# Optimization experiments

Hardware: AMD Instinct MI355X
Metric: run time of the kernel (lower is better)

Reference implementation:

```python
import jax, jax.numpy as jnp
import numpy as np

B, DX, DS, H, K, NSN = 1048576, 32, 16, 128, 64, 4

def setup_inputs() -> dict:
    key = jax.random.key(0)
    ks = jax.random.split(key, 9)
    return {
        "x": jax.random.normal(ks[0], (B, DX), jnp.float32),
        "s": jax.random.normal(ks[1], (B, DS), jnp.float32),
        "hidden": jax.random.normal(ks[2], (B, H), jnp.float32),
        "naive_pred": jax.random.normal(ks[3], (B, 1), jnp.float32),
        # learned parameters
        "centers": jax.random.normal(ks[4], (K, DX), jnp.float32),
        "W_tune": jax.random.normal(ks[5], (H, 1), jnp.float32) * 0.05,
        "b_tune": jnp.zeros((1,), jnp.float32),
        "W_sn": jax.random.normal(ks[6], (NSN, K, DS), jnp.float32) * 0.1,
        "b_sn": jax.random.normal(ks[7], (NSN, K), jnp.float32) * 0.1,
        "running_sn_weight": jnp.full((K, NSN), 1.0 / NSN, jnp.float32),
    }

def reference(x, s, hidden, naive_pred, centers, W_tune, b_tune, W_sn, b_sn, running_sn_weight):
    # tune head: linear -> sigmoid, [B,1]
    x_tune = jax.nn.sigmoid(hidden @ W_tune + b_tune)
    # nearest-centroid clustering: argmin ||x - c_k||^2 (||x||^2 dropped, constant per row)
    dist = jnp.sum(centers * centers, axis=1) - 2.0 * (x @ centers.T)  # [B,K]
    x_cluster = jnp.argmin(dist, axis=1)  # [B] int32
    # sub-networks: per-cluster linear heads on s; gather cluster-indexed weights
    Ws = W_sn[:, x_cluster, :]                                   # [NSN,B,DS] gather
    x_sn = jnp.einsum('nbd,bd->bn', Ws, s) + b_sn[:, x_cluster].T  # [B,NSN]
    # indexed weighted reduction over sub-network outputs
    w = running_sn_weight[x_cluster]                             # [B,NSN] gather
    x_sn_sum = jnp.sum(x_sn * w, axis=1, keepdims=True)          # [B,1]
    out = x_sn_sum + x_tune * (naive_pred - x_sn_sum)
    return out
```

## Files before the change

kernel.cpp:

```cpp
#include <hip/hip_runtime.h>
#include <math.h>

#define DXc 32
#define DSc 16
#define Hc  128
#define Kc  64
#define NSNc 4

__global__ __launch_bounds__(256, 6) void snclust_fused(
    const float* __restrict__ x,
    const float* __restrict__ s,
    const float* __restrict__ hidden,
    const float* __restrict__ naive_pred,
    const float* __restrict__ centers,
    const float* __restrict__ W_tune,
    const float* __restrict__ b_tune,
    const float* __restrict__ W_sn,
    const float* __restrict__ b_sn,
    const float* __restrict__ rsw,
    float* __restrict__ out,
    int n)
{
    __shared__ float sWc[Kc][DSc + 1];
    __shared__ float sbc[Kc];
    __shared__ float sc2[Kc];

    const int tid = threadIdx.x;

    for (int e = tid; e < Kc * DSc; e += 256) {
        const int c = e >> 4;
        const int j = e & 15;
        float acc = 0.f;
#pragma unroll
        for (int nn = 0; nn < NSNc; ++nn)
            acc = fmaf(rsw[c * NSNc + nn], W_sn[(nn * Kc + c) * DSc + j], acc);
        sWc[c][j] = acc;
    }
    if (tid < Kc) {
        const int c = tid;
        float accb = 0.f;
#pragma unroll
        for (int nn = 0; nn < NSNc; ++nn)
            accb = fmaf(rsw[c * NSNc + nn], b_sn[nn * Kc + c], accb);
        sbc[c] = accb;
        float c2 = 0.f;
#pragma unroll
        for (int d = 0; d < DXc; ++d) {
            const float cv = centers[c * DXc + d];
            c2 = fmaf(cv, cv, c2);
        }
        sc2[c] = c2;
    }
    __syncthreads();

    const size_t b = (size_t)blockIdx.x * 256 + tid;
    if (b >= (size_t)n) return;

    float xr[DXc];
    {
        const float4* x4 = reinterpret_cast<const float4*>(x + b * DXc);
#pragma unroll
        for (int i = 0; i < DXc / 4; ++i) {
            const float4 v = x4[i];
            xr[i * 4 + 0] = v.x; xr[i * 4 + 1] = v.y;
            xr[i * 4 + 2] = v.z; xr[i * 4 + 3] = v.w;
        }
    }

    float hacc = 0.f;
    {
        const float4* h4 = reinterpret_cast<const float4*>(hidden + b * Hc);
#pragma unroll 4
        for (int i = 0; i < Hc / 4; ++i) {
            const float4 v = h4[i];
            hacc = fmaf(v.x, W_tune[i * 4 + 0], hacc);
            hacc = fmaf(v.y, W_tune[i * 4 + 1], hacc);
            hacc = fmaf(v.z, W_tune[i * 4 + 2], hacc);
            hacc = fmaf(v.w, W_tune[i * 4 + 3], hacc);
        }
    }
    const float z = hacc + b_tune[0];
    const float x_tune = 1.0f / (1.0f + __expf(-z));

    float4 st[4];
    {
        const float4* s4 = reinterpret_cast<const float4*>(s + b * DSc);
#pragma unroll
        for (int i = 0; i < DSc / 4; ++i)
            st[i] = s4[i];
    }
    const float np_ = naive_pred[b];

    int bestk = 0;
    float bestd = INFINITY;
#pragma unroll 2
    for (int k = 0; k < Kc; ++k) {
        float dot = 0.f;
#pragma unroll
        for (int d = 0; d < DXc; ++d)
            dot = fmaf(xr[d], centers[k * DXc + d], dot);
        const float dist = fmaf(-2.0f, dot, sc2[k]);
        if (dist < bestd) { bestd = dist; bestk = k; }
    }

    float snacc = sbc[bestk];
#pragma unroll
    for (int i = 0; i < DSc / 4; ++i) {
        const float4 v = st[i];
        snacc = fmaf(v.x, sWc[bestk][i * 4 + 0], snacc);
        snacc = fmaf(v.y, sWc[bestk][i * 4 + 1], snacc);
        snacc = fmaf(v.z, sWc[bestk][i * 4 + 2], snacc);
        snacc = fmaf(v.w, sWc[bestk][i * 4 + 3], snacc);
    }

    out[b] = snacc + x_tune * (np_ - snacc);
}

extern "C" void kernel_launch(void* const* d_in, const int* in_sizes, int n_in,
                              void* d_out, int out_size, void* d_ws, size_t ws_size,
                              hipStream_t stream) {
    const float* x          = (const float*)d_in[0];
    const float* s          = (const float*)d_in[1];
    const float* hidden     = (const float*)d_in[2];
    const float* naive_pred = (const float*)d_in[3];
    const float* centers    = (const float*)d_in[4];
    const float* W_tune     = (const float*)d_in[5];
    const float* b_tune     = (const float*)d_in[6];
    const float* W_sn       = (const float*)d_in[7];
    const float* b_sn       = (const float*)d_in[8];
    const float* rsw        = (const float*)d_in[9];
    float* out = (float*)d_out;

    const int n = in_sizes[3];
    const int blocks = (n + 255) / 256;
    snclust_fused<<<blocks, 256, 0, stream>>>(x, s, hidden, naive_pred, centers,
                                              W_tune, b_tune, W_sn, b_sn, rsw,
                                              out, n);
}
```

Measured before the change: 168.8 us.

## Split tune head into coalesced wave-cooperative kernel, feed result via workspace

Moves the hidden@W_tune sigmoid head out of the fused per-row kernel into a separate grid-stride kernel. There, each half-wave reads one 512-byte hidden row with fully coalesced float4 loads and reduces it with shuffles, instead of every thread striding through its own row. The main kernel then reads the precomputed tune value from workspace and defers the s and naive_pred loads until after the argmin loop, which lowers register pressure. The split adds a second launch plus a B-float write and read round-trip, and lowers launch_bounds occupancy from 6 to 4.

```diff
diff --git a/kernel.cpp b/kernel.cpp
--- a/kernel.cpp
+++ b/kernel.cpp
@@ -7,14 +7,64 @@
 #define Kc  64
 #define NSNc 4
 
-__global__ __launch_bounds__(256, 6) void snclust_fused(
+__global__ __launch_bounds__(256, 4) void tune_kernel(
+    const float* __restrict__ hidden,
+    const float* __restrict__ W_tune,
+    const float* __restrict__ b_tune,
+    float* __restrict__ tune,
+    int n)
+{
+    const int lane = threadIdx.x & 63;
+    const int c = lane & 31;
+    const int g = lane >> 5;
+
+    const float4 wt = reinterpret_cast<const float4*>(W_tune)[c];
+    const float bt = b_tune[0];
+
+    const int waveGlobal = (int)((blockIdx.x * 256 + threadIdx.x) >> 6);
+    const int nWaves = (int)((gridDim.x * 256) >> 6);
+    const int nPass = (n + 1) >> 1;
+
+    const float4* h4 = reinterpret_cast<const float4*>(hidden);
+
+    for (int p = waveGlobal; p < nPass; p += 4 * nWaves) {
+        float4 v[4];
+        long long rowk[4];
+#pragma unroll
+        for (int k = 0; k < 4; ++k) {
+            const int pk = p + k * nWaves;
+            const long long row = (long long)2 * pk + g;
+            rowk[k] = row;
+            if (pk < nPass && row < n)
+                v[k] = h4[row * (Hc / 4) + c];
+            else
+                v[k] = make_float4(0.f, 0.f, 0.f, 0.f);
+        }
+#pragma unroll
+        for (int k = 0; k < 4; ++k) {
+            const int pk = p + k * nWaves;
+            if (pk >= nPass) break;
+            float acc = v[k].x * wt.x;
+            acc = fmaf(v[k].y, wt.y, acc);
+            acc = fmaf(v[k].z, wt.z, acc);
+            acc = fmaf(v[k].w, wt.w, acc);
+#pragma unroll
+            for (int m = 1; m < 32; m <<= 1)
+                acc += __shfl_xor(acc, m, 64);
+            if (c == 0 && rowk[k] < n) {
+                const float xt = 1.0f / (1.0f + __expf(-(acc + bt)));
+                tune[rowk[k]] = xt;
+            }
+        }
+    }
+}
+
+__global__ __launch_bounds__(256, 4) void snb_kernel(
     const float* __restrict__ x,
     const float* __restrict__ s,
-    const float* __restrict__ hidden,
     const float* __restrict__ naive_pred,
+    const float* __restrict__ tune,
     const float* __restrict__ centers,
-    const float* __restrict__ W_tune,
-    const float* __restrict__ b_tune,
     const float* __restrict__ W_sn,
     const float* __restrict__ b_sn,
     const float* __restrict__ rsw,
@@ -67,29 +117,7 @@
         }
     }
 
-    float hacc = 0.f;
-    {
-        const float4* h4 = reinterpret_cast<const float4*>(hidden + b * Hc);
-#pragma unroll 4
-        for (int i = 0; i < Hc / 4; ++i) {
-            const float4 v = h4[i];
-            hacc = fmaf(v.x, W_tune[i * 4 + 0], hacc);
-            hacc = fmaf(v.y, W_tune[i * 4 + 1], hacc);
-            hacc = fmaf(v.z, W_tune[i * 4 + 2], hacc);
-            hacc = fmaf(v.w, W_tune[i * 4 + 3], hacc);
-        }
-    }
-    const float z = hacc + b_tune[0];
-    const float x_tune = 1.0f / (1.0f + __expf(-z));
-
-    float4 st[4];
-    {
-        const float4* s4 = reinterpret_cast<const float4*>(s + b * DSc);
-#pragma unroll
-        for (int i = 0; i < DSc / 4; ++i)
-            st[i] = s4[i];
-    }
-    const float np_ = naive_pred[b];
+    const float x_tune = tune[b];
 
     int bestk = 0;
     float bestd = INFINITY;
@@ -104,15 +132,19 @@
     }
 
     float snacc = sbc[bestk];
+    {
+        const float4* s4 = reinterpret_cast<const float4*>(s + b * DSc);
 #pragma unroll
-    for (int i = 0; i < DSc / 4; ++i) {
-        const float4 v = st[i];
-        snacc = fmaf(v.x, sWc[bestk][i * 4 + 0], snacc);
-        snacc = fmaf(v.y, sWc[bestk][i * 4 + 1], snacc);
-        snacc = fmaf(v.z, sWc[bestk][i * 4 + 2], snacc);
-        snacc = fmaf(v.w, sWc[bestk][i * 4 + 3], snacc);
+        for (int i = 0; i < DSc / 4; ++i) {
+            const float4 v = s4[i];
+            snacc = fmaf(v.x, sWc[bestk][i * 4 + 0], snacc);
+            snacc = fmaf(v.y, sWc[bestk][i * 4 + 1], snacc);
+            snacc = fmaf(v.z, sWc[bestk][i * 4 + 2], snacc);
+            snacc = fmaf(v.w, sWc[bestk][i * 4 + 3], snacc);
+        }
     }
 
+    const float np_ = naive_pred[b];
     out[b] = snacc + x_tune * (np_ - snacc);
 }
 
@@ -129,11 +161,14 @@
     const float* W_sn       = (const float*)d_in[7];
     const float* b_sn       = (const float*)d_in[8];
     const float* rsw        = (const float*)d_in[9];
-    float* out = (float*)d_out;
+    float* out  = (float*)d_out;
+    float* tune = (float*)d_ws;
 
     const int n = in_sizes[3];
+
+    tune_kernel<<<2048, 256, 0, stream>>>(hidden, W_tune, b_tune, tune, n);
+
     const int blocks = (n + 255) / 256;
-    snclust_fused<<<blocks, 256, 0, stream>>>(x, s, hidden, naive_pred, centers,
-                                              W_tune, b_tune, W_sn, b_sn, rsw,
-                                              out, n);
+    snb_kernel<<<blocks, 256, 0, stream>>>(x, s, naive_pred, tune, centers,
+                                           W_sn, b_sn, rsw, out, n);
 }
```

Result: slower. 193.0 us (+14.4%).
